# Kernel optimization log

Measured on AMD Instinct MI355X. Metric: run time of the kernel, lower is better.

## Reference

```python
import jax, jax.numpy as jnp
import numpy as np

DIM = 1024
NUM_HEADS = 16
HEAD_DIM = DIM // NUM_HEADS
SCALE = HEAD_DIM ** -0.5


def setup_inputs() -> dict:
    key = jax.random.key(0)
    k_x, k_qw, k_qb, k_pw, k_pb = jax.random.split(key, 5)
    B, N = 4, 4096
    x = jax.random.normal(k_x, (B, N, DIM), dtype=jnp.float32)
    # nn.Linear(dim, 3*dim): weight (out, in), bias (out,)
    s = DIM ** -0.5
    qkv_w = jax.random.uniform(k_qw, (3 * DIM, DIM), jnp.float32, -s, s)
    qkv_b = jax.random.uniform(k_qb, (3 * DIM,), jnp.float32, -s, s)
    proj_w = jax.random.uniform(k_pw, (DIM, DIM), jnp.float32, -s, s)
    proj_b = jax.random.uniform(k_pb, (DIM,), jnp.float32, -s, s)
    return {"x": x, "qkv_w": qkv_w, "qkv_b": qkv_b,
            "proj_w": proj_w, "proj_b": proj_b}


def reference(x, qkv_w, qkv_b, proj_w, proj_b):
    B, N, C = x.shape
    H, D = NUM_HEADS, HEAD_DIM
    # qkv projection: (B,N,3C) -> (B,N,3,H,D)
    qkv = (jnp.einsum('bnc,oc->bno', x, qkv_w) + qkv_b).reshape(B, N, 3, H, D)
    q, k, v = qkv[:, :, 0], qkv[:, :, 1], qkv[:, :, 2]  # each (B,N,H,D)
    # Faithful to source: matmul over the last two dims of (B,N,H,D),
    # i.e. attention scores over the HEAD axis per token -> (B,N,H,H).
    attn = jnp.einsum('bnhd,bngd->bnhg', q, k) * SCALE
    attn = jax.nn.softmax(attn, axis=-1)
    out = jnp.einsum('bnhg,bngd->bnhd', attn, v)      # (B,N,H,D)
    # torch: .transpose(1,2).reshape(B,N,C) -> (B,H,N,D) reshaped to (B,N,C)
    out = out.transpose(0, 2, 1, 3).reshape(B, N, C)
    return jnp.einsum('bnc,oc->bno', out, proj_w) + proj_b
```

## Files before the change

### kernel.cpp

```cpp
#include <hip/hip_runtime.h>
#include <hip/hip_bf16.h>

#define TOK   16384
#define KD    1024
#define NQKV  3072
#define SEQL  4096
#define ATT_SCALE 0.125f

typedef __attribute__((ext_vector_type(4))) float f32x4;
typedef __attribute__((ext_vector_type(8))) short bf16x8;

__device__ __forceinline__ unsigned short f2b(float f){
    union { float f; unsigned u; } x; x.f = f;
    return (unsigned short)((x.u + 0x7FFFu + ((x.u >> 16) & 1u)) >> 16);
}
__device__ __forceinline__ float b2f(unsigned short s){
    union { unsigned u; float f; } x; x.u = ((unsigned)s) << 16;
    return x.f;
}
__device__ __forceinline__ bf16x8 lds8(const unsigned short* p){
    union { uint4 u; bf16x8 v; } t; t.u = *(const uint4*)p; return t.v;
}
__device__ __forceinline__ void glds16(const void* g, void* l){
    __builtin_amdgcn_global_load_lds((const __attribute__((address_space(1))) unsigned*)g,
                                     (__attribute__((address_space(3))) unsigned*)l, 16, 0, 0);
}

__global__ __launch_bounds__(256) void cvt_kernel(const float* __restrict__ in,
                                                  unsigned short* __restrict__ out, int n)
{
    int i = (blockIdx.x * 256 + threadIdx.x) * 8;
    if (i >= n) return;
    float4 a = *(const float4*)(in + i);
    float4 b = *(const float4*)(in + i + 4);
    union { unsigned short u[8]; uint4 v; } t;
    t.u[0]=f2b(a.x); t.u[1]=f2b(a.y); t.u[2]=f2b(a.z); t.u[3]=f2b(a.w);
    t.u[4]=f2b(b.x); t.u[5]=f2b(b.y); t.u[6]=f2b(b.z); t.u[7]=f2b(b.w);
    *(uint4*)(out + i) = t.v;
}

template<bool OUT_BF16>
__global__ __launch_bounds__(512, 2) void gemm256(const unsigned short* __restrict__ A,
        const unsigned short* __restrict__ Bw, const float* __restrict__ bias,
        void* __restrict__ Cp, int Nn)
{
    extern __shared__ unsigned short smem[];
    unsigned short* As = smem;
    unsigned short* Bs = smem + 32768;

    const int tid = threadIdx.x, lane = tid & 63;
    const int w = tid >> 6, wm = w >> 2, wn = w & 3;
    const int rl = lane & 15, kslot = lane >> 4;

    const int gx = gridDim.x;
    const int nwg = gx * gridDim.y;
    int id = blockIdx.y * gx + blockIdx.x;
    id = (id & 7) * (nwg >> 3) + (id >> 3);
    const int cBase = (id % gx) * 256;
    const int mBase = (id / gx) * 256;

    const int u = tid >> 3;
    const int seg8 = ((tid & 7) ^ (u & 7)) * 8;
    const unsigned short* Ag = A  + (size_t)(mBase + u) * KD + seg8;
    const unsigned short* Bg = Bw + (size_t)(cBase + (u >> 4) * 64 + (u & 15)) * KD + seg8;

    const int arow = (wm * 16 + rl) * 64;
    const int brow = (wn * 16 + rl) * 64;
    const int psg0 = (kslot ^ (rl & 7)) * 8;
    const int psg1 = ((kslot + 4) ^ (rl & 7)) * 8;

    f32x4 acc[8][4];
    #pragma unroll
    for (int m = 0; m < 8; m++)
        #pragma unroll
        for (int n = 0; n < 4; n++) acc[m][n] = (f32x4)0.f;

#define STAGE_AH0(bb, kk) { glds16(Ag + (kk),            As + (bb)*16384 + tid*8); \
                            glds16(Ag + 64*KD + (kk),    As + (bb)*16384 + 4096  + tid*8); }
#define STAGE_AH1(bb, kk) { glds16(Ag + 128*KD + (kk),   As + (bb)*16384 + 8192  + tid*8); \
                            glds16(Ag + 192*KD + (kk),   As + (bb)*16384 + 12288 + tid*8); }
#define STAGE_BH0(bb, kk) { glds16(Bg + (kk),            Bs + (bb)*16384 + tid*8); \
                            glds16(Bg + 16*KD + (kk),    Bs + (bb)*16384 + 4096  + tid*8); }
#define STAGE_BH1(bb, kk) { glds16(Bg + 32*KD + (kk),    Bs + (bb)*16384 + 8192  + tid*8); \
                            glds16(Bg + 48*KD + (kk),    Bs + (bb)*16384 + 12288 + tid*8); }

#define RDA(a_, half) { _Pragma("unroll") \
    for (int m = 0; m < 4; m++) { \
        af[m][0] = lds8((a_) + (half)*8192 + arow + m*2048 + psg0); \
        af[m][1] = lds8((a_) + (half)*8192 + arow + m*2048 + psg1); } }
#define RDBP(b_) { _Pragma("unroll") \
    for (int n = 0; n < 2; n++) { \
        bfP[n][0] = lds8((b_) + brow + n*4096 + psg0); \
        bfP[n][1] = lds8((b_) + brow + n*4096 + psg1); } }
#define RDBQ(b_) { _Pragma("unroll") \
    for (int n = 0; n < 2; n++) { \
        bfQ[n][0] = lds8((b_) + brow + (2+n)*4096 + psg0); \
        bfQ[n][1] = lds8((b_) + brow + (2+n)*4096 + psg1); } }

#define MM(mb, nb, BF) { \
    __builtin_amdgcn_s_setprio(1); \
    _Pragma("unroll") \
    for (int m = 0; m < 4; m++) \
        _Pragma("unroll") \
        for (int n = 0; n < 2; n++) { \
            acc[(mb)+m][(nb)+n] = __builtin_amdgcn_mfma_f32_16x16x32_bf16(af[m][0], BF[n][0], acc[(mb)+m][(nb)+n], 0, 0, 0); \
            acc[(mb)+m][(nb)+n] = __builtin_amdgcn_mfma_f32_16x16x32_bf16(af[m][1], BF[n][1], acc[(mb)+m][(nb)+n], 0, 0, 0); } \
    __builtin_amdgcn_s_setprio(0); }

#define VMC(N)  asm volatile("s_waitcnt vmcnt(" #N ")" ::: "memory");
#define LGK(N)  asm volatile("s_waitcnt lgkmcnt(" #N ")" ::: "memory");
#define BAR()   __builtin_amdgcn_s_barrier();

    bf16x8 af[4][2], bfP[2][2], bfQ[2][2];

    STAGE_AH0(0, 0)
    STAGE_BH0(0, 0)
    STAGE_BH1(0, 0)
    STAGE_AH1(0, 0)
    VMC(4)
    BAR()
    RDA(As, 0)
    RDBP(Bs)

    int buf = 0;
    for (int t = 0; t < 15; ++t) {
        const unsigned short* a = As + buf * 16384;
        const unsigned short* b = Bs + buf * 16384;
        const unsigned short* an = As + (buf ^ 1) * 16384;
        const unsigned short* bn = Bs + (buf ^ 1) * 16384;
        const int nk = (t + 1) * 64;
        STAGE_AH0(buf ^ 1, nk)
        VMC(4)
        BAR()
        RDBQ(b)
        LGK(4)
        MM(0, 0, bfP)
        BAR()
        STAGE_BH0(buf ^ 1, nk)
        VMC(4)
        BAR()
        LGK(0)
        MM(0, 2, bfQ)
        RDA(a, 1)
        BAR()
        STAGE_BH1(buf ^ 1, nk)
        BAR()
        LGK(0)
        MM(4, 0, bfP)
        BAR()
        STAGE_AH1(buf ^ 1, nk)
        VMC(4)
        BAR()
        RDBP(bn)
        MM(4, 2, bfQ)
        RDA(an, 0)
        BAR()
        buf ^= 1;
    }
    {
        const unsigned short* a = As + buf * 16384;
        const unsigned short* b = Bs + buf * 16384;
        VMC(2)
        BAR()
        RDBQ(b)
        LGK(4)
        MM(0, 0, bfP)
        VMC(0)
        BAR()
        LGK(0)
        MM(0, 2, bfQ)
        RDA(a, 1)
        LGK(0)
        MM(4, 0, bfP)
        MM(4, 2, bfQ)
    }
#undef STAGE_AH0
#undef STAGE_AH1
#undef STAGE_BH0
#undef STAGE_BH1
#undef RDA
#undef RDBP
#undef RDBQ
#undef MM
#undef VMC
#undef LGK
#undef BAR

    float bv[4];
    #pragma unroll
    for (int n = 0; n < 4; n++) bv[n] = bias[cBase + wn * 64 + n * 16 + rl];
    #pragma unroll
    for (int m = 0; m < 8; m++) {
        #pragma unroll
        for (int i = 0; i < 4; i++) {
            const size_t row = mBase + (m >> 2) * 128 + (m & 3) * 32 + wm * 16 + kslot * 4 + i;
            #pragma unroll
            for (int n = 0; n < 4; n++) {
                const int col = cBase + wn * 64 + n * 16 + rl;
                const float val = acc[m][n][i] + bv[n];
                if (OUT_BF16) ((unsigned short*)Cp)[row * Nn + col] = f2b(val);
                else          ((float*)Cp)[row * Nn + col] = val;
            }
        }
    }
}

__global__ __launch_bounds__(256) void attn_kernel(const unsigned short* __restrict__ qkv,
                                                   unsigned short* __restrict__ outp)
{
    __shared__ __align__(16) unsigned short qs[4][48 * 72];
    __shared__ float ps[4][16 * 17];
    const int tid = threadIdx.x, w = tid >> 6, lane = tid & 63;
    const int t = blockIdx.x * 4 + w;

    const unsigned short* src = qkv + (size_t)t * NQKV;
    #pragma unroll
    for (int i = 0; i < 6; i++) {
        const int e = i * 512 + lane * 8;
        uint4 v = *(const uint4*)(src + e);
        *(uint4*)&qs[w][(e >> 6) * 72 + (e & 63)] = v;
    }
    __syncthreads();

    const int h = lane & 15, g0 = lane >> 4;
    uint4 qv[8];
    #pragma unroll
    for (int i = 0; i < 8; i++) qv[i] = *(const uint4*)&qs[w][h * 72 + i * 8];
    float s[4];
    #pragma unroll
    for (int i = 0; i < 4; i++) {
        const int g = g0 * 4 + i;
        float a = 0.f;
        #pragma unroll
        for (int c = 0; c < 8; c++) {
            uint4 kv = *(const uint4*)&qs[w][(16 + g) * 72 + c * 8];
            uint qa[4] = {qv[c].x, qv[c].y, qv[c].z, qv[c].w};
            uint ka[4] = {kv.x, kv.y, kv.z, kv.w};
            #pragma unroll
            for (int uu = 0; uu < 4; uu++) {
                a += b2f((unsigned short)qa[uu]) * b2f((unsigned short)ka[uu]);
                a += b2f((unsigned short)(qa[uu] >> 16)) * b2f((unsigned short)(ka[uu] >> 16));
            }
        }
        s[i] = a * ATT_SCALE;
    }
    float mx = fmaxf(fmaxf(s[0], s[1]), fmaxf(s[2], s[3]));
    mx = fmaxf(mx, __shfl_xor(mx, 16, 64));
    mx = fmaxf(mx, __shfl_xor(mx, 32, 64));
    float p[4], smv = 0.f;
    #pragma unroll
    for (int i = 0; i < 4; i++) { p[i] = __expf(s[i] - mx); smv += p[i]; }
    smv += __shfl_xor(smv, 16, 64);
    smv += __shfl_xor(smv, 32, 64);
    const float inv = 1.f / smv;
    #pragma unroll
    for (int i = 0; i < 4; i++) ps[w][h * 17 + g0 * 4 + i] = p[i] * inv;
    __syncthreads();

    const int h2 = lane >> 2, db = (lane & 3) * 16;
    float pr[16];
    #pragma unroll
    for (int g = 0; g < 16; g++) pr[g] = ps[w][h2 * 17 + g];
    float acc[16];
    #pragma unroll
    for (int j = 0; j < 16; j++) acc[j] = 0.f;
    #pragma unroll
    for (int g = 0; g < 16; g++) {
        const unsigned short* vp = &qs[w][(32 + g) * 72 + db];
        uint4 v0 = *(const uint4*)vp;
        uint4 v1 = *(const uint4*)(vp + 8);
        const float pg = pr[g];
        uint va[8] = {v0.x, v0.y, v0.z, v0.w, v1.x, v1.y, v1.z, v1.w};
        #pragma unroll
        for (int uu = 0; uu < 8; uu++) {
            acc[2*uu]   += pg * b2f((unsigned short)va[uu]);
            acc[2*uu+1] += pg * b2f((unsigned short)(va[uu] >> 16));
        }
    }
    const int b = t >> 12, n = t & 4095;
    const int n1 = h2 * 256 + (n >> 4);
    const int c0 = (n & 15) * 64 + db;
    union { unsigned short u[16]; uint4 v[2]; } st;
    #pragma unroll
    for (int j = 0; j < 16; j++) st.u[j] = f2b(acc[j]);
    unsigned short* dst = outp + ((size_t)(b * SEQL + n1)) * 1024 + c0;
    *(uint4*)dst       = st.v[0];
    *(uint4*)(dst + 8) = st.v[1];
}

extern "C" void kernel_launch(void* const* d_in, const int* in_sizes, int n_in,
                              void* d_out, int out_size, void* d_ws, size_t ws_size,
                              hipStream_t stream)
{
    const float* x      = (const float*)d_in[0];
    const float* qkv_w  = (const float*)d_in[1];
    const float* qkv_b  = (const float*)d_in[2];
    const float* proj_w = (const float*)d_in[3];
    const float* proj_b = (const float*)d_in[4];

    unsigned short* xb  = (unsigned short*)d_ws;
    unsigned short* qkv = xb + (size_t)TOK * KD;
    unsigned short* qwb = qkv + (size_t)TOK * NQKV;
    unsigned short* pwb = qwb + (size_t)NQKV * KD;
    unsigned short* att = xb;

    hipFuncSetAttribute(reinterpret_cast<const void*>(&gemm256<true>),
                        hipFuncAttributeMaxDynamicSharedMemorySize, 131072);
    hipFuncSetAttribute(reinterpret_cast<const void*>(&gemm256<false>),
                        hipFuncAttributeMaxDynamicSharedMemorySize, 131072);

    cvt_kernel<<<dim3(TOK * KD / 2048), dim3(256), 0, stream>>>(x, xb, TOK * KD);
    cvt_kernel<<<dim3(NQKV * KD / 2048), dim3(256), 0, stream>>>(qkv_w, qwb, NQKV * KD);
    cvt_kernel<<<dim3(KD * KD / 2048), dim3(256), 0, stream>>>(proj_w, pwb, KD * KD);

    gemm256<true><<<dim3(NQKV / 256, TOK / 256), dim3(512), 131072, stream>>>(
        xb, qwb, qkv_b, qkv, NQKV);
    attn_kernel<<<dim3(TOK / 4), dim3(256), 0, stream>>>(qkv, att);
    gemm256<false><<<dim3(KD / 256, TOK / 256), dim3(512), 131072, stream>>>(
        att, pwb, proj_b, (float*)d_out, KD);
}
```

Baseline: 225.6 us.

## Restructure GEMM main loop into 8-phase ping-pong schedule with deeper prefetch

Rewrites the double-buffered GEMM K-loop as an unrolled-by-two ping-pong schedule. Global-to-LDS staging of the next tile is spread across four MFMA phases per tile, and each phase is bracketed by barriers, in the style of an 8-wave ping-pong pipeline. The aim is more overlap of global loads, LDS reads and MFMA work by keeping about one and a half tiles of loads in flight. In exchange it adds more barriers per iteration and full lgkmcnt(0) waits, which may serialise LDS reads with the math.

```diff
diff --git a/kernel.cpp b/kernel.cpp
--- a/kernel.cpp
+++ b/kernel.cpp
@@ -108,70 +108,60 @@
     __builtin_amdgcn_s_setprio(0); }
 
 #define VMC(N)  asm volatile("s_waitcnt vmcnt(" #N ")" ::: "memory");
-#define LGK(N)  asm volatile("s_waitcnt lgkmcnt(" #N ")" ::: "memory");
-#define BAR()   __builtin_amdgcn_s_barrier();
+#define LGK0    asm volatile("s_waitcnt lgkmcnt(0)" ::: "memory");
+#define BARR    __builtin_amdgcn_s_barrier();
 
     bf16x8 af[4][2], bfP[2][2], bfQ[2][2];
-
-    STAGE_AH0(0, 0)
-    STAGE_BH0(0, 0)
-    STAGE_BH1(0, 0)
-    STAGE_AH1(0, 0)
-    VMC(4)
-    BAR()
-    RDA(As, 0)
-    RDBP(Bs)
-
-    int buf = 0;
-    for (int t = 0; t < 15; ++t) {
-        const unsigned short* a = As + buf * 16384;
-        const unsigned short* b = Bs + buf * 16384;
-        const unsigned short* an = As + (buf ^ 1) * 16384;
-        const unsigned short* bn = Bs + (buf ^ 1) * 16384;
-        const int nk = (t + 1) * 64;
-        STAGE_AH0(buf ^ 1, nk)
-        VMC(4)
-        BAR()
-        RDBQ(b)
-        LGK(4)
-        MM(0, 0, bfP)
-        BAR()
-        STAGE_BH0(buf ^ 1, nk)
-        VMC(4)
-        BAR()
-        LGK(0)
-        MM(0, 2, bfQ)
-        RDA(a, 1)
-        BAR()
-        STAGE_BH1(buf ^ 1, nk)
-        BAR()
-        LGK(0)
-        MM(4, 0, bfP)
-        BAR()
-        STAGE_AH1(buf ^ 1, nk)
-        VMC(4)
-        BAR()
-        RDBP(bn)
-        MM(4, 2, bfQ)
-        RDA(an, 0)
-        BAR()
-        buf ^= 1;
+    const unsigned short* a0 = As;
+    const unsigned short* b0 = Bs;
+    const unsigned short* a1 = As + 16384;
+    const unsigned short* b1 = Bs + 16384;
+
+    STAGE_AH0(0, 0) STAGE_BH0(0, 0) STAGE_BH1(0, 0) STAGE_AH1(0, 0)
+    STAGE_AH0(1, 64) STAGE_BH0(1, 64) STAGE_BH1(1, 64)
+    VMC(6)
+    BARR
+
+    for (int J = 0; J < 7; ++J) {
+        const int k1 = (2*J + 1) * 64, k2 = (2*J + 2) * 64, k3 = (2*J + 3) * 64;
+        RDA(a0, 0) RDBP(b0)
+        STAGE_AH1(1, k1)
+        BARR LGK0 MM(0, 0, bfP) BARR
+        RDBQ(b0)
+        STAGE_AH0(0, k2)
+        BARR LGK0 MM(0, 2, bfQ) BARR
+        RDA(a0, 1)
+        STAGE_BH0(0, k2)
+        BARR LGK0 MM(4, 0, bfP) BARR
+        STAGE_BH1(0, k2)
+        BARR MM(4, 2, bfQ) VMC(6) BARR
+        RDA(a1, 0) RDBP(b1)
+        STAGE_AH1(0, k2)
+        BARR LGK0 MM(0, 0, bfP) BARR
+        RDBQ(b1)
+        STAGE_AH0(1, k3)
+        BARR LGK0 MM(0, 2, bfQ) BARR
+        RDA(a1, 1)
+        STAGE_BH0(1, k3)
+        BARR LGK0 MM(4, 0, bfP) BARR
+        STAGE_BH1(1, k3)
+        BARR MM(4, 2, bfQ) VMC(6) BARR
     }
     {
-        const unsigned short* a = As + buf * 16384;
-        const unsigned short* b = Bs + buf * 16384;
-        VMC(2)
-        BAR()
-        RDBQ(b)
-        LGK(4)
-        MM(0, 0, bfP)
-        VMC(0)
-        BAR()
-        LGK(0)
-        MM(0, 2, bfQ)
-        RDA(a, 1)
-        LGK(0)
-        MM(4, 0, bfP)
+        RDA(a0, 0) RDBP(b0)
+        STAGE_AH1(1, 15 * 64)
+        BARR LGK0 MM(0, 0, bfP) BARR
+        RDBQ(b0)
+        BARR LGK0 MM(0, 2, bfQ) BARR
+        RDA(a0, 1)
+        BARR LGK0 MM(4, 0, bfP) BARR
+        BARR MM(4, 2, bfQ) VMC(4) BARR
+        RDA(a1, 0) RDBP(b1)
+        BARR LGK0 MM(0, 0, bfP) VMC(2) BARR
+        RDBQ(b1)
+        BARR LGK0 MM(0, 2, bfQ) VMC(0) BARR
+        RDA(a1, 1)
+        BARR LGK0 MM(4, 0, bfP) BARR
         MM(4, 2, bfQ)
     }
 #undef STAGE_AH0
@@ -183,8 +173,8 @@
 #undef RDBQ
 #undef MM
 #undef VMC
-#undef LGK
-#undef BAR
+#undef LGK0
+#undef BARR
 
     float bv[4];
     #pragma unroll
```

After: 243.0 us. 7.7% more time.
